# Performance work log

Hardware: AMD Instinct MI355X
Metric: run time of the kernel (lower is better)

Reference implementation:

```python
import jax, jax.numpy as jnp
import numpy as np
import math

NUM_HEADS = 16
NUM_BUCKETS = 32
MAX_DISTANCE = 128
ALPHA = 32.0


def _rel_bucket(rel_pos):
    # bidirectional T5-style bucketing
    nb = NUM_BUCKETS // 2
    buckets = (rel_pos > 0).astype(jnp.int32) * nb
    rel_pos = jnp.abs(rel_pos)
    max_exact = nb // 2
    is_small = rel_pos < max_exact
    large = max_exact + (
        jnp.log(rel_pos.astype(jnp.float32) / max_exact + 1e-06)
        / math.log(MAX_DISTANCE / max_exact)
        * (nb - max_exact)
    ).astype(jnp.int32)
    large = jnp.minimum(large, nb - 1)
    return buckets + jnp.where(is_small, rel_pos, large)


def setup_inputs() -> dict:
    key = jax.random.key(0)
    ks = jax.random.split(key, 12)
    T, B, E = 1024, 4, 1024
    hd = E // NUM_HEADS
    s = 0.02
    f32 = jnp.float32
    return {
        "query": jax.random.normal(ks[0], (T, B, E), f32),
        "q_w": jax.random.normal(ks[1], (E, E), f32) * s,
        "q_b": jnp.zeros((E,), f32),
        "k_w": jax.random.normal(ks[2], (E, E), f32) * s,
        "k_b": jnp.zeros((E,), f32),
        "v_w": jax.random.normal(ks[3], (E, E), f32) * s,
        "v_b": jnp.zeros((E,), f32),
        "out_w": jax.random.normal(ks[4], (E, E), f32) * s,
        "out_b": jnp.zeros((E,), f32),
        "rel_emb": jax.random.normal(ks[5], (NUM_BUCKETS, NUM_HEADS), f32) * 0.1,
        "grep_w": jax.random.normal(ks[6], (hd, 8), f32) * s,
        "grep_b": jnp.zeros((8,), f32),
        "grep_a": jnp.ones((1, NUM_HEADS, 1, 1), f32),
        "bias_k": jax.random.normal(ks[7], (1, 1, E), f32) * s,
        "bias_v": jax.random.normal(ks[8], (1, 1, E), f32) * s,
    }


def reference(query, q_w, q_b, k_w, k_b, v_w, v_b, out_w, out_b,
              rel_emb, grep_w, grep_b, grep_a, bias_k, bias_v):
    tgt_len, bsz, embed_dim = query.shape
    nh = NUM_HEADS
    hd = embed_dim // nh
    scaling = hd ** (-0.5)

    # projections (self-attention: q, k, v all from query)
    q = query @ q_w + q_b
    k = query @ k_w + k_b
    v = query @ v_w + v_b
    q = q * scaling / ALPHA

    # bias_kv concat along sequence axis
    k = jnp.concatenate([k, jnp.tile(bias_k, (1, bsz, 1))], axis=0)
    v = jnp.concatenate([v, jnp.tile(bias_v, (1, bsz, 1))], axis=0)

    # faithful to source layout (including its (bsz,tgt,nh,hd)->(bsz*nh,tgt,hd) reshape)
    q = jnp.transpose(q.reshape(tgt_len, bsz, nh, hd), (1, 0, 2, 3)).reshape(bsz * nh, tgt_len, hd)
    k = jnp.transpose(k.reshape(-1, bsz, nh, hd), (1, 0, 2, 3)).reshape(bsz * nh, -1, hd)
    v = jnp.transpose(v.reshape(-1, bsz, nh, hd), (1, 0, 2, 3)).reshape(bsz * nh, -1, hd)
    src_len = k.shape[1]

    # [B*H, T, S]
    attn_weights = jnp.einsum("bth,bsh->bts", q, k)

    # T5-style relative position bias
    rel_pos = jnp.arange(src_len)[None, :] - jnp.arange(tgt_len)[:, None]
    buckets = _rel_bucket(rel_pos)                        # [T, S]
    pb = rel_emb[buckets]                                 # [T, S, H]
    pb = jnp.transpose(pb, (2, 0, 1))                     # [H, T, S]
    pb = jnp.tile(pb[None], (bsz, 1, 1, 1)).reshape(bsz * nh, tgt_len, src_len)

    # GRU-style gating of the position bias
    query_layer = q.reshape(bsz, nh, tgt_len, hd) * ALPHA / scaling
    gate = jax.nn.sigmoid((query_layer @ grep_w + grep_b).sum(-1, keepdims=True))
    gate = (gate * grep_a).reshape(bsz * nh, tgt_len, 1)
    attn_weights = attn_weights + gate * pb

    probs = jax.nn.softmax(attn_weights, axis=-1)
    attn = jnp.einsum("bts,bsh->bth", probs, v)           # [B*H, T, hd]
    attn = attn.reshape(bsz, nh, tgt_len, hd)
    attn = jnp.transpose(attn, (2, 0, 1, 3)).reshape(tgt_len, bsz, embed_dim)
    return attn @ out_w + out_b
```

## Files before the change

### kernel.cpp

```cpp
#include <hip/hip_runtime.h>
#include <stdint.h>

typedef unsigned short u16;
typedef unsigned int   u32;
typedef __attribute__((ext_vector_type(4)))  float f32x4;
typedef __attribute__((ext_vector_type(16))) float f32x16;
typedef __attribute__((ext_vector_type(8)))  short short8;
typedef __attribute__((ext_vector_type(8)))  u16   u16x8;
typedef __attribute__((ext_vector_type(4)))  u16   u16x4;
typedef __attribute__((ext_vector_type(4)))  u32   u32x4;
typedef __attribute__((ext_vector_type(4)))  float fv4;

#define T_LEN 1024
#define EMB   1024
#define SPAD  1088
#define LOG2E 1.44269504f

#define OFF_QX   (0ull)
#define OFF_VT   (0ull)
#define OFF_WT   (8912896ull)
#define OFF_QB   (17301504ull)
#define OFF_KB   (25690112ull)
#define OFF_VB   (34603008ull)
#define OFF_AT   (34603008ull)
#define OFF_GATE (43515904ull)
#define OFF_PB   (43778048ull)
#define OFF_AUX  (43909120ull)

__device__ __forceinline__ u16 f2bf(float f) {
  uint32_t u = __builtin_bit_cast(uint32_t, f);
  u += 0x7FFFu + ((u >> 16) & 1u);
  return (u16)(u >> 16);
}
__device__ __forceinline__ float bf2f(u16 s) {
  uint32_t u = ((uint32_t)s) << 16;
  return __builtin_bit_cast(float, u);
}
__device__ __forceinline__ void gld_lds16(const void* gp, void* lp) {
  __builtin_amdgcn_global_load_lds(
      (const __attribute__((address_space(1))) uint32_t*)(uintptr_t)(gp),
      (__attribute__((address_space(3))) uint32_t*)(uintptr_t)(lp),
      16, 0, 0);
}

__global__ void k_prep(const float* __restrict__ q, u16* __restrict__ qx,
                       const float* __restrict__ w0, const float* __restrict__ w1,
                       const float* __restrict__ w2, const float* __restrict__ w3,
                       u16* __restrict__ wt,
                       const float* __restrict__ rel_emb, float* __restrict__ pbtab,
                       const float* __restrict__ grep_w, const float* __restrict__ grep_b,
                       float* __restrict__ aux) {
  __shared__ float tile[32][33];
  const int bid = blockIdx.x, tid = threadIdx.x;
  if (bid < 4096) {
    int i = bid * 256 + tid;
    fv4 v = *((const fv4*)q + i);
    u16x4 o = { f2bf(v[0]), f2bf(v[1]), f2bf(v[2]), f2bf(v[3]) };
    *((u16x4*)qx + i) = o;
  } else if (bid < 8192) {
    int b2 = bid - 4096;
    int z = b2 >> 10, xy = b2 & 1023;
    int r0 = (xy >> 5) * 32, c0 = (xy & 31) * 32;
    const float* w = (z == 0) ? w0 : (z == 1) ? w1 : (z == 2) ? w2 : w3;
    int tx = tid & 31, ty = tid >> 5;
    #pragma unroll
    for (int j = 0; j < 32; j += 8)
      tile[ty + j][tx] = w[(size_t)(r0 + ty + j) * EMB + c0 + tx];
    __syncthreads();
    u16* o = wt + (size_t)z * EMB * EMB;
    #pragma unroll
    for (int j = 0; j < 32; j += 8)
      o[(size_t)(c0 + ty + j) * EMB + r0 + tx] = f2bf(tile[tx][ty + j]);
  } else {
    int i = (bid - 8192) * 256 + tid;
    int rel = 1024 - i;
    int bucket = (rel > 0) ? 16 : 0;
    int r = rel < 0 ? -rel : rel;
    int bidx;
    if (r < 8) bidx = r;
    else {
      float lf = __logf((float)r / 8.0f + 1e-6f) * (1.0f / logf(16.0f)) * 8.0f;
      int large = 8 + (int)lf;
      bidx = large < 15 ? large : 15;
    }
    bucket += bidx;
    #pragma unroll
    for (int hh = 0; hh < 16; ++hh) pbtab[hh * 2048 + i] = rel_emb[bucket * 16 + hh] * LOG2E;
    if (bid == 8192) {
      if (tid < 64) {
        float s = 0.f;
        #pragma unroll
        for (int j = 0; j < 8; ++j) s += grep_w[tid * 8 + j];
        aux[tid] = s;
      } else if (tid == 64) {
        float s = 0.f;
        #pragma unroll
        for (int j = 0; j < 8; ++j) s += grep_b[j];
        aux[64] = s;
      }
    }
  }
}

__device__ __forceinline__ void gemm_tile(const u16* __restrict__ A, const u16* __restrict__ Bt,
                                          int m0, int n0, u16* As, u16* Bs, f32x4 acc[4][4]) {
  const int tid = threadIdx.x;
  const int lane = tid & 63, wid = tid >> 6;
  const int wm = wid >> 1, wn = wid & 1;
  const int l15 = lane & 15, l4 = lane >> 4;
  for (int kt = 0; kt < EMB; kt += 32) {
    #pragma unroll
    for (int i = 0; i < 2; ++i) {
      int cw = wid * 64 + i * 256;
      int c = cw + lane;
      int row = c >> 2, cb = c & 3;
      gld_lds16(A  + (size_t)(m0 + row) * EMB + kt + cb * 8, (char*)As + (size_t)cw * 16);
      gld_lds16(Bt + (size_t)(n0 + row) * EMB + kt + cb * 8, (char*)Bs + (size_t)cw * 16);
    }
    __syncthreads();
    short8 a[4], b[4];
    #pragma unroll
    for (int f = 0; f < 4; ++f) {
      a[f] = *(const short8*)(As + (wm * 64 + f * 16 + l15) * 32 + l4 * 8);
      b[f] = *(const short8*)(Bs + (wn * 64 + f * 16 + l15) * 32 + l4 * 8);
    }
    #pragma unroll
    for (int mi = 0; mi < 4; ++mi)
      #pragma unroll
      for (int ni = 0; ni < 4; ++ni)
        acc[mi][ni] = __builtin_amdgcn_mfma_f32_16x16x32_bf16(a[mi], b[ni], acc[mi][ni], 0, 0, 0);
    __syncthreads();
  }
}

__global__ __launch_bounds__(256, 2) void k_qkv_gemm(const u16* __restrict__ qx, const u16* __restrict__ wt,
    const float* __restrict__ qbias, const float* __restrict__ kbias, const float* __restrict__ vbias,
    u16* __restrict__ qb, u16* __restrict__ kb, u16* __restrict__ vb) {
  __shared__ u16 lds[8192];
  f32x4 acc[4][4];
  #pragma unroll
  for (int i = 0; i < 4; ++i)
    #pragma unroll
    for (int j = 0; j < 4; ++j) acc[i][j] = (f32x4){0.f, 0.f, 0.f, 0.f};
  const int m0 = blockIdx.y * 128, n0g = blockIdx.x * 128;
  gemm_tile(qx, wt, m0, n0g, lds, lds + 4096, acc);
  const int z = n0g >> 10;
  const float* bias = (z == 0) ? qbias : (z == 1) ? kbias : vbias;
  const int lane = threadIdx.x & 63, wid = threadIdx.x >> 6;
  const int wm = wid >> 1, wn = wid & 1, l15 = lane & 15, l4 = lane >> 4;
  #pragma unroll
  for (int ni = 0; ni < 4; ++ni) {
    int colg = n0g + wn * 64 + ni * 16 + l15;
    int col = colg & 1023;
    float bv = bias[col];
    int h = col >> 6, d = col & 63;
    #pragma unroll
    for (int mi = 0; mi < 4; ++mi) {
      #pragma unroll
      for (int r = 0; r < 4; ++r) {
        int row = m0 + wm * 64 + mi * 16 + l4 * 4 + r;
        int t = row >> 2, b = row & 3;
        float v = acc[mi][ni][r] + bv;
        if (z == 0) {
          int x = b * 16 + (t >> 6), u = ((t & 63) << 4) + h;
          qb[((size_t)x * 1024 + u) * 64 + d] = f2bf(v * (LOG2E / 256.0f));
        } else {
          int w = t * 16 + h;
          int j = w / 1025;
          int u = w - j * 1025;
          int x = b * 16 + j;
          if (z == 1) kb[((size_t)x * SPAD + u) * 64 + d] = f2bf(v);
          else        vb[((size_t)x * SPAD + u) * 64 + d] = f2bf(v);
        }
      }
    }
  }
}

__global__ void k_mid(const u16* __restrict__ vb, u16* __restrict__ vt, u16* __restrict__ kb,
                      const float* __restrict__ bias_k, const float* __restrict__ bias_v,
                      const u16* __restrict__ qb, const float* __restrict__ aux,
                      const float* __restrict__ grep_a, float* __restrict__ gate) {
  __shared__ u16 t[64][72];
  const int bid = blockIdx.x, tid = threadIdx.x;
  if (bid < 1088) {
    const int x = bid / 17, uc = bid - (bid / 17) * 17;
    const int u0 = uc * 64;
    const int ur = tid >> 2, c0 = (tid & 3) * 16;
    const u16* src = vb + ((size_t)x * SPAD + u0 + ur) * 64 + c0;
    u16x8 a0 = *(const u16x8*)(src);
    u16x8 a1 = *(const u16x8*)(src + 8);
    const int ug = u0 + ur;
    if ((x & 15) == 15 && ug >= 1009 && ug <= 1024) {
      const float* bs = bias_v + (ug - 1009) * 64 + c0;
      #pragma unroll
      for (int i = 0; i < 8; ++i) { a0[i] = f2bf(bs[i]); a1[i] = f2bf(bs[8 + i]); }
    }
    *(u16x8*)(&t[ur][c0]) = a0;
    *(u16x8*)(&t[ur][c0 + 8]) = a1;
    __syncthreads();
    const int d = tid >> 2, j = tid & 3;
    u16x8 o0, o1;
    #pragma unroll
    for (int i = 0; i < 8; ++i) o0[i] = t[j * 16 + i][d];
    #pragma unroll
    for (int i = 0; i < 8; ++i) o1[i] = t[j * 16 + 8 + i][d];
    u16* dst = vt + ((size_t)x * 64 + d) * SPAD + u0 + j * 16;
    *(u16x8*)(dst) = o0;
    *(u16x8*)(dst + 8) = o1;
    if ((x & 15) == 15 && uc == 16) {
      int k = tid * 4;
      int hh = k >> 6, dd = k & 63;
      u16x4 kv;
      #pragma unroll
      for (int e = 0; e < 4; ++e) kv[e] = f2bf(bias_k[hh * 64 + dd + e]);
      *(u16x4*)(kb + ((size_t)x * SPAD + 1009 + hh) * 64 + dd) = kv;
    }
  } else {
    int gb = bid - 1088;
    int lane = tid & 63, wid = tid >> 6;
    int row0 = (gb * 4 + wid) * 8;
    int sub = lane >> 3, d0 = (lane & 7) * 8;
    int item = row0 + sub;
    u16x8 q8 = *(const u16x8*)(qb + (size_t)item * 64 + d0);
    float acc = 0.f;
    #pragma unroll
    for (int j = 0; j < 8; ++j) acc += bf2f(q8[j]) * aux[d0 + j];
    acc += __shfl_xor(acc, 1);
    acc += __shfl_xor(acc, 2);
    acc += __shfl_xor(acc, 4);
    if ((lane & 7) == 0) {
      float v = acc * (256.0f / LOG2E) + aux[64];
      float s = 1.0f / (1.0f + __expf(-v));
      gate[item] = s * grep_a[(item >> 10) & 15];
    }
  }
}

__global__ __launch_bounds__(256, 2) void k_attn(const u16* __restrict__ qb, const u16* __restrict__ kb,
    const u16* __restrict__ vt, const float* __restrict__ gate, const float* __restrict__ pbt,
    u16* __restrict__ at) {
  __shared__ float pb_s[2048];
  const int tid = threadIdx.x, lane = tid & 63, wid = tid >> 6;
  const int l31 = lane & 31, l5 = lane >> 5;
  const int bid = blockIdx.x;
  const int x = (bid & 7) + ((bid >> 6) << 3);
  const int tblk = (bid >> 3) & 7;
  const int h = x & 15, b = x >> 4;
  const int T = tblk * 128 + wid * 32 + l31;

  #pragma unroll
  for (int i = 0; i < 2; ++i) {
    int idx = (tid + i * 256) * 4;
    *(fv4*)(pb_s + idx) = *(const fv4*)(pbt + (size_t)h * 2048 + idx);
  }

  short8 qf[4];
  #pragma unroll
  for (int c = 0; c < 4; ++c)
    qf[c] = *(const short8*)(qb + ((size_t)x * 1024 + T) * 64 + c * 16 + l5 * 8);
  const float g = gate[(size_t)x * 1024 + T];

  const u16* kbx = kb + (size_t)x * SPAD * 64;
  const u16* vtx = vt + (size_t)x * 64 * SPAD;

  f32x16 O0 = {}, O1 = {};
  float lsum = 0.f;

  short8 kA[2][4], kB[2][4];
  #pragma unroll
  for (int ss = 0; ss < 2; ++ss)
    #pragma unroll
    for (int c = 0; c < 4; ++c)
      kA[ss][c] = *(const short8*)(kbx + (size_t)(ss * 32 + l31) * 64 + c * 16 + l5 * 8);
  __syncthreads();

  auto step = [&](short8 (&ka)[2][4], short8 (&kn)[2][4], int ic, bool pf) {
    const int s0 = ic * 64;
    short8 va[2][4];
    #pragma unroll
    for (int ds = 0; ds < 2; ++ds)
      #pragma unroll
      for (int c = 0; c < 4; ++c)
        va[ds][c] = *(const short8*)(vtx + (size_t)(ds * 32 + l31) * SPAD + s0 + c * 16 + l5 * 8);
    if (pf) {
      const int sn = s0 + 64;
      #pragma unroll
      for (int ss = 0; ss < 2; ++ss)
        #pragma unroll
        for (int c = 0; c < 4; ++c)
          kn[ss][c] = *(const short8*)(kbx + (size_t)(sn + ss * 32 + l31) * 64 + c * 16 + l5 * 8);
    }
    f32x16 sc0 = {}, sc1 = {};
    __builtin_amdgcn_s_setprio(1);
    #pragma unroll
    for (int c = 0; c < 4; ++c) {
      sc0 = __builtin_amdgcn_mfma_f32_32x32x16_bf16(ka[0][c], qf[c], sc0, 0, 0, 0);
      sc1 = __builtin_amdgcn_mfma_f32_32x32x16_bf16(ka[1][c], qf[c], sc1, 0, 0, 0);
    }
    __builtin_amdgcn_s_setprio(0);
    const int base = 1024 + T - s0;
    u32 pk[16];
    #pragma unroll
    for (int r = 0; r < 16; r += 2) {
      int soff = (r & 3) + 8 * (r >> 2) + 4 * l5;
      float p0 = exp2f(sc0[r]     + g * pb_s[base - soff]);
      float p1 = exp2f(sc0[r + 1] + g * pb_s[base - soff - 1]);
      lsum += p0 + p1;
      pk[r >> 1] = (__builtin_bit_cast(u32, p1) & 0xFFFF0000u) |
                   (__builtin_bit_cast(u32, p0) >> 16);
    }
    #pragma unroll
    for (int r = 0; r < 16; r += 2) {
      int soff = 32 + (r & 3) + 8 * (r >> 2) + 4 * l5;
      float p0 = exp2f(sc1[r]     + g * pb_s[base - soff]);
      float p1 = exp2f(sc1[r + 1] + g * pb_s[base - soff - 1]);
      lsum += p0 + p1;
      pk[8 + (r >> 1)] = (__builtin_bit_cast(u32, p1) & 0xFFFF0000u) |
                         (__builtin_bit_cast(u32, p0) >> 16);
    }
    __builtin_amdgcn_s_setprio(1);
    #pragma unroll
    for (int ss = 0; ss < 2; ++ss) {
      u32 a0 = pk[ss * 8 + 0], a1 = pk[ss * 8 + 1];
      u32 b0 = pk[ss * 8 + 2], b1 = pk[ss * 8 + 3];
      asm volatile("v_permlane32_swap_b32 %0, %1" : "+v"(a0), "+v"(b0));
      asm volatile("v_permlane32_swap_b32 %0, %1" : "+v"(a1), "+v"(b1));
      u32x4 f0v = { a0, a1, b0, b1 };
      short8 pf0 = __builtin_bit_cast(short8, f0v);
      O0 = __builtin_amdgcn_mfma_f32_32x32x16_bf16(va[0][ss * 2], pf0, O0, 0, 0, 0);
      O1 = __builtin_amdgcn_mfma_f32_32x32x16_bf16(va[1][ss * 2], pf0, O1, 0, 0, 0);
      u32 c0 = pk[ss * 8 + 4], c1 = pk[ss * 8 + 5];
      u32 d0 = pk[ss * 8 + 6], d1 = pk[ss * 8 + 7];
      asm volatile("v_permlane32_swap_b32 %0, %1" : "+v"(c0), "+v"(d0));
      asm volatile("v_permlane32_swap_b32 %0, %1" : "+v"(c1), "+v"(d1));
      u32x4 f1v = { c0, c1, d0, d1 };
      short8 pf1 = __builtin_bit_cast(short8, f1v);
      O0 = __builtin_amdgcn_mfma_f32_32x32x16_bf16(va[0][ss * 2 + 1], pf1, O0, 0, 0, 0);
      O1 = __builtin_amdgcn_mfma_f32_32x32x16_bf16(va[1][ss * 2 + 1], pf1, O1, 0, 0, 0);
    }
    __builtin_amdgcn_s_setprio(0);
  };

  #pragma unroll 1
  for (int ic = 0; ic < 16; ic += 2) {
    step(kA, kB, ic, true);
    step(kB, kA, ic + 1, ic + 1 < 15);
  }

  float dot = 0.f;
  #pragma unroll
  for (int c = 0; c < 4; ++c) {
    short8 kt = *(const short8*)(kbx + (size_t)1024 * 64 + c * 16 + l5 * 8);
    #pragma unroll
    for (int j = 0; j < 8; ++j)
      dot += bf2f((u16)qf[c][j]) * bf2f((u16)kt[j]);
  }
  dot += __shfl_xor(dot, 32);
  float se = dot + g * pb_s[T];
  float p_t = exp2f(se);
  lsum += __shfl_xor(lsum, 32);
  float linv = 1.0f / (lsum + p_t);

  #pragma unroll
  for (int ds = 0; ds < 2; ++ds) {
    #pragma unroll
    for (int q2 = 0; q2 < 4; ++q2) {
      int d0 = ds * 32 + q2 * 8 + l5 * 4;
      u16x4 ov;
      #pragma unroll
      for (int e = 0; e < 4; ++e) {
        float vtl = bf2f(vtx[(size_t)(d0 + e) * SPAD + 1024]);
        float o = ((ds ? O1[q2 * 4 + e] : O0[q2 * 4 + e]) + p_t * vtl) * linv;
        ov[e] = f2bf(o);
      }
      *(u16x4*)(at + ((size_t)(T * 4 + b)) * 1024 + h * 64 + d0) = ov;
    }
  }
}

__global__ __launch_bounds__(256, 2) void k_out_gemm(const u16* __restrict__ at, const u16* __restrict__ wt3,
                                                     const float* __restrict__ obias, float* __restrict__ out) {
  __shared__ u16 lds[8192];
  f32x4 acc[4][4];
  #pragma unroll
  for (int i = 0; i < 4; ++i)
    #pragma unroll
    for (int j = 0; j < 4; ++j) acc[i][j] = (f32x4){0.f, 0.f, 0.f, 0.f};
  const int m0 = blockIdx.y * 128, n0 = blockIdx.x * 128;
  gemm_tile(at, wt3, m0, n0, lds, lds + 4096, acc);
  const int lane = threadIdx.x & 63, wid = threadIdx.x >> 6;
  const int wm = wid >> 1, wn = wid & 1, l15 = lane & 15, l4 = lane >> 4;
  #pragma unroll
  for (int ni = 0; ni < 4; ++ni) {
    int col = n0 + wn * 64 + ni * 16 + l15;
    float bv = obias[col];
    #pragma unroll
    for (int mi = 0; mi < 4; ++mi) {
      #pragma unroll
      for (int r = 0; r < 4; ++r) {
        int row = m0 + wm * 64 + mi * 16 + l4 * 4 + r;
        out[(size_t)row * 1024 + col] = acc[mi][ni][r] + bv;
      }
    }
  }
}

extern "C" void kernel_launch(void* const* d_in, const int* in_sizes, int n_in,
                              void* d_out, int out_size, void* d_ws, size_t ws_size,
                              hipStream_t stream) {
  const float* query   = (const float*)d_in[0];
  const float* q_w     = (const float*)d_in[1];
  const float* q_b     = (const float*)d_in[2];
  const float* k_w     = (const float*)d_in[3];
  const float* k_b     = (const float*)d_in[4];
  const float* v_w     = (const float*)d_in[5];
  const float* v_b     = (const float*)d_in[6];
  const float* out_w   = (const float*)d_in[7];
  const float* out_b   = (const float*)d_in[8];
  const float* rel_emb = (const float*)d_in[9];
  const float* grep_w  = (const float*)d_in[10];
  const float* grep_b  = (const float*)d_in[11];
  const float* grep_a  = (const float*)d_in[12];
  const float* bias_k  = (const float*)d_in[13];
  const float* bias_v  = (const float*)d_in[14];
  char* ws = (char*)d_ws;
  u16*   qx  = (u16*)(ws + OFF_QX);
  u16*   vt  = (u16*)(ws + OFF_VT);
  u16*   wt  = (u16*)(ws + OFF_WT);
  u16*   qb  = (u16*)(ws + OFF_QB);
  u16*   kb  = (u16*)(ws + OFF_KB);
  u16*   vb  = (u16*)(ws + OFF_VB);
  u16*   at  = (u16*)(ws + OFF_AT);
  float* gate = (float*)(ws + OFF_GATE);
  float* pbt  = (float*)(ws + OFF_PB);
  float* aux  = (float*)(ws + OFF_AUX);
  float* out  = (float*)d_out;

  k_prep<<<dim3(8200), dim3(256), 0, stream>>>(query, qx, q_w, k_w, v_w, out_w, wt,
                                               rel_emb, pbt, grep_w, grep_b, aux);
  k_qkv_gemm<<<dim3(24, 32), dim3(256), 0, stream>>>(qx, wt, q_b, k_b, v_b, qb, kb, vb);
  k_mid<<<dim3(3136), dim3(256), 0, stream>>>(vb, vt, kb, bias_k, bias_v, qb, aux, grep_a, gate);
  k_attn<<<dim3(512), dim3(256), 0, stream>>>(qb, kb, vt, gate, pbt, at);
  k_out_gemm<<<dim3(8, 32), dim3(256), 0, stream>>>(at, wt + (size_t)3 * EMB * EMB, out_b, out);
}
```

Measured before the change: 234.4 us.

## Split attention KV range across wave pairs and skip bias gathers for far chunks

The attention kernel now gives each pair of waves the same 32 query rows and splits the 1024 key positions in half between them. The partial outputs and row sums are combined through shared memory, so the grid doubles to 1024 blocks and the launch bound rises to 4 blocks per SM for more parallelism and occupancy. Key chunks far from the diagonal, where the relative-position bucket is constant, use a single precomputed bias value instead of per-element LDS gathers. The explicit K-register double-buffer prefetch is removed, which may expose more load latency, and the LDS combine adds a barrier and extra shared-memory traffic.

```diff
diff --git a/kernel.cpp b/kernel.cpp
--- a/kernel.cpp
+++ b/kernel.cpp
@@ -237,17 +237,21 @@
   }
 }
 
-__global__ __launch_bounds__(256, 2) void k_attn(const u16* __restrict__ qb, const u16* __restrict__ kb,
+__global__ __launch_bounds__(256, 4) void k_attn(const u16* __restrict__ qb, const u16* __restrict__ kb,
     const u16* __restrict__ vt, const float* __restrict__ gate, const float* __restrict__ pbt,
     u16* __restrict__ at) {
   __shared__ float pb_s[2048];
+  __shared__ float comb[2][32][64];
+  __shared__ float comb_l[64];
   const int tid = threadIdx.x, lane = tid & 63, wid = tid >> 6;
   const int l31 = lane & 31, l5 = lane >> 5;
+  const int rg = wid >> 1, sh = wid & 1;
   const int bid = blockIdx.x;
-  const int x = (bid & 7) + ((bid >> 6) << 3);
-  const int tblk = (bid >> 3) & 7;
+  const int x = (bid & 7) + ((bid >> 7) << 3);
+  const int tblk = (bid >> 3) & 15;
   const int h = x & 15, b = x >> 4;
-  const int T = tblk * 128 + wid * 32 + l31;
+  const int T0w = tblk * 64 + rg * 32;
+  const int T = T0w + l31;
 
   #pragma unroll
   for (int i = 0; i < 2; ++i) {
@@ -266,31 +270,26 @@
 
   f32x16 O0 = {}, O1 = {};
   float lsum = 0.f;
-
-  short8 kA[2][4], kB[2][4];
-  #pragma unroll
-  for (int ss = 0; ss < 2; ++ss)
-    #pragma unroll
-    for (int c = 0; c < 4; ++c)
-      kA[ss][c] = *(const short8*)(kbx + (size_t)(ss * 32 + l31) * 64 + c * 16 + l5 * 8);
   __syncthreads();
-
-  auto step = [&](short8 (&ka)[2][4], short8 (&kn)[2][4], int ic, bool pf) {
+  const float gFn = g * pb_s[1300];
+  const float gFp = g * pb_s[800];
+
+  #pragma unroll 1
+  for (int i = 0; i < 8; ++i) {
+    const int ic = sh * 8 + i;
     const int s0 = ic * 64;
+    short8 ka[2][4];
+    #pragma unroll
+    for (int ss = 0; ss < 2; ++ss)
+      #pragma unroll
+      for (int c = 0; c < 4; ++c)
+        ka[ss][c] = *(const short8*)(kbx + (size_t)(s0 + ss * 32 + l31) * 64 + c * 16 + l5 * 8);
     short8 va[2][4];
     #pragma unroll
     for (int ds = 0; ds < 2; ++ds)
       #pragma unroll
       for (int c = 0; c < 4; ++c)
         va[ds][c] = *(const short8*)(vtx + (size_t)(ds * 32 + l31) * SPAD + s0 + c * 16 + l5 * 8);
-    if (pf) {
-      const int sn = s0 + 64;
-      #pragma unroll
-      for (int ss = 0; ss < 2; ++ss)
-        #pragma unroll
-        for (int c = 0; c < 4; ++c)
-          kn[ss][c] = *(const short8*)(kbx + (size_t)(sn + ss * 32 + l31) * 64 + c * 16 + l5 * 8);
-    }
     f32x16 sc0 = {}, sc1 = {};
     __builtin_amdgcn_s_setprio(1);
     #pragma unroll
@@ -301,23 +300,43 @@
     __builtin_amdgcn_s_setprio(0);
     const int base = 1024 + T - s0;
     u32 pk[16];
-    #pragma unroll
-    for (int r = 0; r < 16; r += 2) {
-      int soff = (r & 3) + 8 * (r >> 2) + 4 * l5;
-      float p0 = exp2f(sc0[r]     + g * pb_s[base - soff]);
-      float p1 = exp2f(sc0[r + 1] + g * pb_s[base - soff - 1]);
-      lsum += p0 + p1;
-      pk[r >> 1] = (__builtin_bit_cast(u32, p1) & 0xFFFF0000u) |
-                   (__builtin_bit_cast(u32, p0) >> 16);
-    }
-    #pragma unroll
-    for (int r = 0; r < 16; r += 2) {
-      int soff = 32 + (r & 3) + 8 * (r >> 2) + 4 * l5;
-      float p0 = exp2f(sc1[r]     + g * pb_s[base - soff]);
-      float p1 = exp2f(sc1[r + 1] + g * pb_s[base - soff - 1]);
-      lsum += p0 + p1;
-      pk[8 + (r >> 1)] = (__builtin_bit_cast(u32, p1) & 0xFFFF0000u) |
-                         (__builtin_bit_cast(u32, p0) >> 16);
+    const bool farN = (s0 <= T0w - 191);
+    const bool farP = (s0 >= T0w + 159);
+    if (farN | farP) {
+      const float gf = farN ? gFn : gFp;
+      #pragma unroll
+      for (int r = 0; r < 16; r += 2) {
+        float p0 = exp2f(sc0[r] + gf), p1 = exp2f(sc0[r + 1] + gf);
+        lsum += p0 + p1;
+        pk[r >> 1] = (__builtin_bit_cast(u32, p1) & 0xFFFF0000u) |
+                     (__builtin_bit_cast(u32, p0) >> 16);
+      }
+      #pragma unroll
+      for (int r = 0; r < 16; r += 2) {
+        float p0 = exp2f(sc1[r] + gf), p1 = exp2f(sc1[r + 1] + gf);
+        lsum += p0 + p1;
+        pk[8 + (r >> 1)] = (__builtin_bit_cast(u32, p1) & 0xFFFF0000u) |
+                           (__builtin_bit_cast(u32, p0) >> 16);
+      }
+    } else {
+      #pragma unroll
+      for (int r = 0; r < 16; r += 2) {
+        int soff = (r & 3) + 8 * (r >> 2) + 4 * l5;
+        float p0 = exp2f(sc0[r]     + g * pb_s[base - soff]);
+        float p1 = exp2f(sc0[r + 1] + g * pb_s[base - soff - 1]);
+        lsum += p0 + p1;
+        pk[r >> 1] = (__builtin_bit_cast(u32, p1) & 0xFFFF0000u) |
+                     (__builtin_bit_cast(u32, p0) >> 16);
+      }
+      #pragma unroll
+      for (int r = 0; r < 16; r += 2) {
+        int soff = 32 + (r & 3) + 8 * (r >> 2) + 4 * l5;
+        float p0 = exp2f(sc1[r]     + g * pb_s[base - soff]);
+        float p1 = exp2f(sc1[r + 1] + g * pb_s[base - soff - 1]);
+        lsum += p0 + p1;
+        pk[8 + (r >> 1)] = (__builtin_bit_cast(u32, p1) & 0xFFFF0000u) |
+                           (__builtin_bit_cast(u32, p0) >> 16);
+      }
     }
     __builtin_amdgcn_s_setprio(1);
     #pragma unroll
@@ -340,41 +359,64 @@
       O1 = __builtin_amdgcn_mfma_f32_32x32x16_bf16(va[1][ss * 2 + 1], pf1, O1, 0, 0, 0);
     }
     __builtin_amdgcn_s_setprio(0);
-  };
-
-  #pragma unroll 1
-  for (int ic = 0; ic < 16; ic += 2) {
-    step(kA, kB, ic, true);
-    step(kB, kA, ic + 1, ic + 1 < 15);
-  }
-
-  float dot = 0.f;
-  #pragma unroll
-  for (int c = 0; c < 4; ++c) {
-    short8 kt = *(const short8*)(kbx + (size_t)1024 * 64 + c * 16 + l5 * 8);
-    #pragma unroll
-    for (int j = 0; j < 8; ++j)
-      dot += bf2f((u16)qf[c][j]) * bf2f((u16)kt[j]);
-  }
-  dot += __shfl_xor(dot, 32);
-  float se = dot + g * pb_s[T];
-  float p_t = exp2f(se);
+  }
+
   lsum += __shfl_xor(lsum, 32);
-  float linv = 1.0f / (lsum + p_t);
-
-  #pragma unroll
-  for (int ds = 0; ds < 2; ++ds) {
-    #pragma unroll
-    for (int q2 = 0; q2 < 4; ++q2) {
-      int d0 = ds * 32 + q2 * 8 + l5 * 4;
-      u16x4 ov;
-      #pragma unroll
-      for (int e = 0; e < 4; ++e) {
-        float vtl = bf2f(vtx[(size_t)(d0 + e) * SPAD + 1024]);
-        float o = ((ds ? O1[q2 * 4 + e] : O0[q2 * 4 + e]) + p_t * vtl) * linv;
-        ov[e] = f2bf(o);
-      }
-      *(u16x4*)(at + ((size_t)(T * 4 + b)) * 1024 + h * 64 + d0) = ov;
+
+  if (sh) {
+    float dot = 0.f;
+    #pragma unroll
+    for (int c = 0; c < 4; ++c) {
+      short8 kt = *(const short8*)(kbx + (size_t)1024 * 64 + c * 16 + l5 * 8);
+      #pragma unroll
+      for (int j = 0; j < 8; ++j)
+        dot += bf2f((u16)qf[c][j]) * bf2f((u16)kt[j]);
+    }
+    dot += __shfl_xor(dot, 32);
+    float p_t = exp2f(dot + g * pb_s[T]);
+    lsum += p_t;
+    #pragma unroll
+    for (int ds = 0; ds < 2; ++ds)
+      #pragma unroll
+      for (int q2 = 0; q2 < 4; ++q2) {
+        int d0 = ds * 32 + q2 * 8 + l5 * 4;
+        #pragma unroll
+        for (int e = 0; e < 4; ++e) {
+          float vtl = bf2f(vtx[(size_t)(d0 + e) * SPAD + 1024]);
+          if (ds) O1[q2 * 4 + e] += p_t * vtl; else O0[q2 * 4 + e] += p_t * vtl;
+        }
+      }
+    #pragma unroll
+    for (int ds = 0; ds < 2; ++ds)
+      #pragma unroll
+      for (int q2 = 0; q2 < 4; ++q2) {
+        int d0 = ds * 32 + q2 * 8 + l5 * 4;
+        int dsw = d0 ^ ((l31 & 15) << 2);
+        f32x4 v;
+        #pragma unroll
+        for (int e = 0; e < 4; ++e) v[e] = ds ? O1[q2 * 4 + e] : O0[q2 * 4 + e];
+        *(f32x4*)(&comb[rg][l31][dsw]) = v;
+      }
+    if (l5 == 0) comb_l[rg * 32 + l31] = lsum;
+  }
+  __syncthreads();
+  if (!sh) {
+    const float linv = 1.0f / (lsum + comb_l[rg * 32 + l31]);
+    #pragma unroll
+    for (int ds = 0; ds < 2; ++ds) {
+      #pragma unroll
+      for (int q2 = 0; q2 < 4; ++q2) {
+        int d0 = ds * 32 + q2 * 8 + l5 * 4;
+        int dsw = d0 ^ ((l31 & 15) << 2);
+        f32x4 pv = *(const f32x4*)(&comb[rg][l31][dsw]);
+        u16x4 ov;
+        #pragma unroll
+        for (int e = 0; e < 4; ++e) {
+          float o = ((ds ? O1[q2 * 4 + e] : O0[q2 * 4 + e]) + pv[e]) * linv;
+          ov[e] = f2bf(o);
+        }
+        *(u16x4*)(at + ((size_t)(T * 4 + b)) * 1024 + h * 64 + d0) = ov;
+      }
     }
   }
 }
@@ -441,6 +483,6 @@
                                                rel_emb, pbt, grep_w, grep_b, aux);
   k_qkv_gemm<<<dim3(24, 32), dim3(256), 0, stream>>>(qx, wt, q_b, k_b, v_b, qb, kb, vb);
   k_mid<<<dim3(3136), dim3(256), 0, stream>>>(vb, vt, kb, bias_k, bias_v, qb, aux, grep_a, gate);
-  k_attn<<<dim3(512), dim3(256), 0, stream>>>(qb, kb, vt, gate, pbt, at);
+  k_attn<<<dim3(1024), dim3(256), 0, stream>>>(qb, kb, vt, gate, pbt, at);
   k_out_gemm<<<dim3(8, 32), dim3(256), 0, stream>>>(at, wt + (size_t)3 * EMB * EMB, out_b, out);
 }
```

Measured after the change: 273.5 us. 16.7% more time.
